# Optimization experiments

Hardware: AMD Instinct MI355X
Metric: run time of the kernel (lower is better)

The kernel has to match this reference:

```python
import jax, jax.numpy as jnp
import numpy as np

EPS = 1e-12  # keras K.l2_normalize epsilon


def _l2_normalize(v, axis):
    return v * jax.lax.rsqrt(jnp.maximum(jnp.sum(v * v, axis=axis, keepdims=True), EPS))


def setup_inputs() -> dict:
    key = jax.random.key(0)
    k1, k2, k3, k4 = jax.random.split(key, 4)
    B, T, D, K, O = 32, 1024, 512, 64, 1024
    x = jax.random.normal(k1, (B, T, D), dtype=jnp.float32)
    weight = jax.random.normal(k2, (D, K), dtype=jnp.float32) * (1.0 / np.sqrt(D))
    bias = jnp.zeros((K,), dtype=jnp.float32)
    centers = jax.random.normal(k3, (K, D), dtype=jnp.float32)
    reduc_dim = jax.random.normal(k4, (D * K, O), dtype=jnp.float32) * 0.01
    return {"x": x, "weight": weight, "bias": bias, "centers": centers, "reduc_dim": reduc_dim}


def reference(x, weight, bias, centers, reduc_dim):
    # x: [B,T,D], weight: [D,K], bias: [K]
    # soft assignment: softmax over centers
    a = jax.nn.softmax(jnp.einsum('btd,dk->btk', x, weight) + bias, axis=-1)  # [B,T,K]
    # aggregate descriptors per center: batch_dot over time axis -> [B,K,D]
    x_agg = jnp.einsum('btk,btd->bkd', a, x)
    # total soft weight per center: [B,K]
    sum_w = jnp.sum(a, axis=1)
    # residual vs centers, broadcast: [B,K,D]
    full = x_agg - sum_w[:, :, None] * centers[None, :, :]
    # intra-normalize per center vector
    full = _l2_normalize(full, axis=-1)
    B = x.shape[0]
    full = full.reshape(B, -1)  # [B, K*D]
    full = _l2_normalize(full, axis=-1)
    return full @ reduc_dim  # [B, output_dim]
```

## Files before the change

### kernel.cpp

```cpp
#include <hip/hip_runtime.h>
#include <math.h>

#define TT 1024
#define DD 512
#define KK 64
#define OO 1024
#define EPSF 1e-12f


__global__ void nv_kzero(float* __restrict__ p) {
  p[blockIdx.x * 256 + threadIdx.x] = 0.f;
}

__global__ __launch_bounds__(256) void nv_k1(
    const float* __restrict__ x, const float* __restrict__ weight,
    const float* __restrict__ bias, float* __restrict__ a_out,
    float* __restrict__ sum_w) {
  const int b = blockIdx.y;
  const int t0 = blockIdx.x * 64;
  const int tid = threadIdx.x;
  const int tx = tid & 15, ty = tid >> 4;
  const int r0 = ty * 4, c0 = tx * 4;

  __shared__ float xs[64 * 68];
  __shared__ float wsm[64 * 64];

  float acc[4][4] = {};

  for (int kk = 0; kk < DD; kk += 64) {
    __syncthreads();
#pragma unroll
    for (int it = 0; it < 4; ++it) {
      int f4 = it * 256 + tid;
      int r = f4 >> 4, d4 = (f4 & 15) << 2;
      *(float4*)(xs + r * 68 + d4) =
          *(const float4*)(x + (size_t)(b * TT + t0 + r) * DD + kk + d4);
    }
#pragma unroll
    for (int it = 0; it < 4; ++it) {
      int f4 = it * 256 + tid;
      int i = f4 >> 4, c4 = (f4 & 15) << 2;
      *(float4*)(wsm + i * 64 + c4) =
          *(const float4*)(weight + (size_t)(kk + i) * KK + c4);
    }
    __syncthreads();
#pragma unroll
    for (int i = 0; i < 64; i += 4) {
      float4 xv[4], wv[4];
#pragma unroll
      for (int j = 0; j < 4; ++j) xv[j] = *(const float4*)(xs + (r0 + j) * 68 + i);
#pragma unroll
      for (int ii = 0; ii < 4; ++ii) wv[ii] = *(const float4*)(wsm + (i + ii) * 64 + c0);
#pragma unroll
      for (int j = 0; j < 4; ++j) {
        acc[j][0] = fmaf(xv[j].x, wv[0].x, acc[j][0]);
        acc[j][1] = fmaf(xv[j].x, wv[0].y, acc[j][1]);
        acc[j][2] = fmaf(xv[j].x, wv[0].z, acc[j][2]);
        acc[j][3] = fmaf(xv[j].x, wv[0].w, acc[j][3]);
        acc[j][0] = fmaf(xv[j].y, wv[1].x, acc[j][0]);
        acc[j][1] = fmaf(xv[j].y, wv[1].y, acc[j][1]);
        acc[j][2] = fmaf(xv[j].y, wv[1].z, acc[j][2]);
        acc[j][3] = fmaf(xv[j].y, wv[1].w, acc[j][3]);
        acc[j][0] = fmaf(xv[j].z, wv[2].x, acc[j][0]);
        acc[j][1] = fmaf(xv[j].z, wv[2].y, acc[j][1]);
        acc[j][2] = fmaf(xv[j].z, wv[2].z, acc[j][2]);
        acc[j][3] = fmaf(xv[j].z, wv[2].w, acc[j][3]);
        acc[j][0] = fmaf(xv[j].w, wv[3].x, acc[j][0]);
        acc[j][1] = fmaf(xv[j].w, wv[3].y, acc[j][1]);
        acc[j][2] = fmaf(xv[j].w, wv[3].z, acc[j][2]);
        acc[j][3] = fmaf(xv[j].w, wv[3].w, acc[j][3]);
      }
    }
  }

  float4 bs = *(const float4*)(bias + c0);
  float swp0 = 0.f, swp1 = 0.f, swp2 = 0.f, swp3 = 0.f;
#pragma unroll
  for (int j = 0; j < 4; ++j) {
    float l0 = acc[j][0] + bs.x, l1 = acc[j][1] + bs.y;
    float l2 = acc[j][2] + bs.z, l3 = acc[j][3] + bs.w;
    float m = fmaxf(fmaxf(l0, l1), fmaxf(l2, l3));
#pragma unroll
    for (int s = 1; s <= 8; s <<= 1) m = fmaxf(m, __shfl_xor(m, s));
    float e0 = __expf(l0 - m), e1 = __expf(l1 - m);
    float e2 = __expf(l2 - m), e3 = __expf(l3 - m);
    float sum = e0 + e1 + e2 + e3;
#pragma unroll
    for (int s = 1; s <= 8; s <<= 1) sum += __shfl_xor(sum, s);
    float inv = 1.f / sum;
    float4 o = make_float4(e0 * inv, e1 * inv, e2 * inv, e3 * inv);
    swp0 += o.x; swp1 += o.y; swp2 += o.z; swp3 += o.w;
    *(float4*)(a_out + (size_t)(b * TT + t0 + r0 + j) * KK + c0) = o;
  }
  __syncthreads();
  *(float4*)(wsm + tid * 4) = make_float4(swp0, swp1, swp2, swp3);
  __syncthreads();
  if (tid < 64) {
    int txx = tid >> 2, cc = tid & 3;
    float s = 0.f;
#pragma unroll
    for (int g = 0; g < 16; ++g) s += wsm[(g * 16 + txx) * 4 + cc];
    atomicAdd(sum_w + b * KK + txx * 4 + cc, s);
  }
}

__global__ __launch_bounds__(256) void nv_k2(
    const float* __restrict__ a_in, const float* __restrict__ x,
    float* __restrict__ xaggP) {
  const int d_base = blockIdx.x * 64;
  const int b = blockIdx.y;
  const int split = blockIdx.z;
  const int tid = threadIdx.x;
  const int tx = tid & 15, ty = tid >> 4;
  const int r0 = ty * 4, c0 = tx * 4;

  __shared__ float as[64 * 64];
  __shared__ float xsm[64 * 64];

  float acc[4][4] = {};

  const int tbeg = split * 256;
  for (int t0 = tbeg; t0 < tbeg + 256; t0 += 64) {
    __syncthreads();
#pragma unroll
    for (int it = 0; it < 4; ++it) {
      int f4 = it * 256 + tid;
      int tt = f4 >> 4, c4 = (f4 & 15) << 2;
      *(float4*)(as + tt * 64 + c4) =
          *(const float4*)(a_in + (size_t)(b * TT + t0 + tt) * KK + c4);
      *(float4*)(xsm + tt * 64 + c4) =
          *(const float4*)(x + (size_t)(b * TT + t0 + tt) * DD + d_base + c4);
    }
    __syncthreads();
#pragma unroll 8
    for (int tt = 0; tt < 64; ++tt) {
      float4 av = *(const float4*)(as + tt * 64 + r0);
      float4 xv = *(const float4*)(xsm + tt * 64 + c0);
      acc[0][0] = fmaf(av.x, xv.x, acc[0][0]);
      acc[0][1] = fmaf(av.x, xv.y, acc[0][1]);
      acc[0][2] = fmaf(av.x, xv.z, acc[0][2]);
      acc[0][3] = fmaf(av.x, xv.w, acc[0][3]);
      acc[1][0] = fmaf(av.y, xv.x, acc[1][0]);
      acc[1][1] = fmaf(av.y, xv.y, acc[1][1]);
      acc[1][2] = fmaf(av.y, xv.z, acc[1][2]);
      acc[1][3] = fmaf(av.y, xv.w, acc[1][3]);
      acc[2][0] = fmaf(av.z, xv.x, acc[2][0]);
      acc[2][1] = fmaf(av.z, xv.y, acc[2][1]);
      acc[2][2] = fmaf(av.z, xv.z, acc[2][2]);
      acc[2][3] = fmaf(av.z, xv.w, acc[2][3]);
      acc[3][0] = fmaf(av.w, xv.x, acc[3][0]);
      acc[3][1] = fmaf(av.w, xv.y, acc[3][1]);
      acc[3][2] = fmaf(av.w, xv.z, acc[3][2]);
      acc[3][3] = fmaf(av.w, xv.w, acc[3][3]);
    }
  }
#pragma unroll
  for (int j = 0; j < 4; ++j) {
    *(float4*)(xaggP + ((size_t)((split * 32 + b) * KK + r0 + j)) * DD + d_base + c0) =
        make_float4(acc[j][0], acc[j][1], acc[j][2], acc[j][3]);
  }
}

__global__ __launch_bounds__(128) void nv_k3a(
    const float* __restrict__ xaggP, float* __restrict__ full,
    const float* __restrict__ centers, const float* __restrict__ sum_w,
    float* __restrict__ s1) {
  const int k = blockIdx.x, b = blockIdx.y;
  const int tid = threadIdx.x;
  const float sw = sum_w[b * KK + k];
  float4 v = make_float4(0.f, 0.f, 0.f, 0.f);
#pragma unroll
  for (int sp = 0; sp < 4; ++sp) {
    float4 p = *((const float4*)(xaggP + (size_t)((sp * 32 + b) * KK + k) * DD) + tid);
    v.x += p.x; v.y += p.y; v.z += p.z; v.w += p.w;
  }
  float4 c = *((const float4*)(centers + (size_t)k * DD) + tid);
  v.x = fmaf(-sw, c.x, v.x);
  v.y = fmaf(-sw, c.y, v.y);
  v.z = fmaf(-sw, c.z, v.z);
  v.w = fmaf(-sw, c.w, v.w);
  *((float4*)(full + (size_t)(b * KK + k) * DD) + tid) = v;
  float ss = v.x * v.x + v.y * v.y + v.z * v.z + v.w * v.w;
#pragma unroll
  for (int s = 1; s <= 32; s <<= 1) ss += __shfl_xor(ss, s);
  __shared__ float red[2];
  if ((tid & 63) == 0) red[tid >> 6] = ss;
  __syncthreads();
  if (tid == 0) s1[b * KK + k] = red[0] + red[1];
}

__global__ __launch_bounds__(64) void nv_k3b(const float* __restrict__ s1,
                                             float* __restrict__ scale) {
  const int b = blockIdx.x, k = threadIdx.x;
  float r = s1[b * KK + k];
  float d1 = fmaxf(r, EPSF);
  float s2 = r / d1;
#pragma unroll
  for (int s = 1; s <= 32; s <<= 1) s2 += __shfl_xor(s2, s);
  scale[b * KK + k] = rsqrtf(d1) * rsqrtf(fmaxf(s2, EPSF));
}

__global__ __launch_bounds__(128) void nv_k3c(float* __restrict__ full,
                                              const float* __restrict__ scale) {
  const int blk = blockIdx.x;
  const float sc = scale[blk];
  float4* p = (float4*)(full + (size_t)blk * DD) + threadIdx.x;
  float4 v = *p;
  v.x *= sc; v.y *= sc; v.z *= sc; v.w *= sc;
  *p = v;
}

__global__ __launch_bounds__(256) void nv_k4(
    const float* __restrict__ full, const float* __restrict__ reduc,
    float* __restrict__ outP) {
  const int c_base = blockIdx.x * 64;
  const int r_base = blockIdx.y * 512;
  const int tid = threadIdx.x;
  const int tx = tid & 15;
  const int ty = (tid >> 4) & 3;
  const int tz = tid >> 6;
  const int c0 = c_base + tx * 4;

  __shared__ float As[32 * 256];

  float acc[8][4] = {};

  for (int ch = 0; ch < 2; ++ch) {
    const int rch = r_base + ch * 256;
    __syncthreads();
#pragma unroll
    for (int it = 0; it < 8; ++it) {
      int f4 = it * 256 + tid;
      int bb = f4 >> 6, rr4 = (f4 & 63) << 2;
      *(float4*)(As + bb * 256 + rr4) =
          *(const float4*)(full + (size_t)bb * 32768 + rch + rr4);
    }
    __syncthreads();
#pragma unroll 4
    for (int i = 0; i < 16; ++i) {
      const int rl = i * 16 + ty * 4;
      float wv[4][4];
#pragma unroll
      for (int j = 0; j < 4; ++j) {
        float4 w = *(const float4*)(reduc + (size_t)(rch + rl + j) * OO + c0);
        wv[j][0] = w.x; wv[j][1] = w.y; wv[j][2] = w.z; wv[j][3] = w.w;
      }
#pragma unroll
      for (int bb = 0; bb < 8; ++bb) {
        float4 a4 = *(const float4*)(As + (tz * 8 + bb) * 256 + rl);
        float a_[4] = {a4.x, a4.y, a4.z, a4.w};
#pragma unroll
        for (int j = 0; j < 4; ++j) {
          acc[bb][0] = fmaf(a_[j], wv[j][0], acc[bb][0]);
          acc[bb][1] = fmaf(a_[j], wv[j][1], acc[bb][1]);
          acc[bb][2] = fmaf(a_[j], wv[j][2], acc[bb][2]);
          acc[bb][3] = fmaf(a_[j], wv[j][3], acc[bb][3]);
        }
      }
    }
  }

#pragma unroll
  for (int bb = 0; bb < 8; ++bb) {
    float4 v = make_float4(acc[bb][0], acc[bb][1], acc[bb][2], acc[bb][3]);
    v.x += __shfl_xor(v.x, 16); v.x += __shfl_xor(v.x, 32);
    v.y += __shfl_xor(v.y, 16); v.y += __shfl_xor(v.y, 32);
    v.z += __shfl_xor(v.z, 16); v.z += __shfl_xor(v.z, 32);
    v.w += __shfl_xor(v.w, 16); v.w += __shfl_xor(v.w, 32);
    if (ty == 0) {
      *(float4*)(outP + (size_t)(blockIdx.y * 32 + tz * 8 + bb) * OO + c0) = v;
    }
  }
}

__global__ __launch_bounds__(256) void nv_k5(const float* __restrict__ outP,
                                             float* __restrict__ out) {
  const int idx = blockIdx.x * 256 + threadIdx.x;
  float s = 0.f;
#pragma unroll 8
  for (int sp = 0; sp < 64; ++sp) s += outP[(size_t)sp * 32768 + idx];
  out[idx] = s;
}

extern "C" void kernel_launch(void* const* d_in, const int* in_sizes, int n_in,
                              void* d_out, int out_size, void* d_ws, size_t ws_size,
                              hipStream_t stream) {
  const float* x = (const float*)d_in[0];
  const float* weight = (const float*)d_in[1];
  const float* bias = (const float*)d_in[2];
  const float* centers = (const float*)d_in[3];
  const float* reduc = (const float*)d_in[4];
  float* out = (float*)d_out;
  float* ws = (float*)d_ws;

  float* a = ws;
  float* full = ws;
  float* xaggP = ws + 2097152;
  float* outP = ws + 2097152;
  float* sum_w = ws + 6291456;
  float* s1 = sum_w + 2048;
  float* scale = sum_w + 4096;

  nv_kzero<<<8, 256, 0, stream>>>(sum_w);
  nv_k1<<<dim3(16, 32), 256, 0, stream>>>(x, weight, bias, a, sum_w);
  nv_k2<<<dim3(8, 32, 4), 256, 0, stream>>>(a, x, xaggP);
  nv_k3a<<<dim3(64, 32), 128, 0, stream>>>(xaggP, full, centers, sum_w, s1);
  nv_k3b<<<32, 64, 0, stream>>>(s1, scale);
  nv_k3c<<<2048, 128, 0, stream>>>(full, scale);
  nv_k4<<<dim3(16, 64), 256, 0, stream>>>(full, reduc, outP);
  nv_k5<<<128, 256, 0, stream>>>(outP, out);
}
```

Measured before the change: 314.8 us.

## Use bf16 MFMA for assignment logits and aggregation GEMMs with transposed bf16 activations

Rewrites the logits GEMM and the soft-assignment aggregation GEMM to use bf16 MFMA 16x16x32 instructions instead of scalar FP32 FMAs. The weight is pre-converted and transposed to bf16, and x is converted on the fly with XOR-swizzled shared memory. Assignments are written transposed in bf16, and the time split for aggregation drops from 4 to 2. The aim is to cut compute time and halve the assignment traffic, at the cost of reduced precision in the logits and aggregation.

```diff
diff --git a/kernel.cpp b/kernel.cpp
--- a/kernel.cpp
+++ b/kernel.cpp
@@ -7,158 +7,218 @@
 #define OO 1024
 #define EPSF 1e-12f
 
+typedef __attribute__((ext_vector_type(8))) short bf16x8;
+typedef __attribute__((ext_vector_type(4))) float f32x4;
+
+__device__ __forceinline__ ushort f2bf(float f) {
+  unsigned u = __float_as_uint(f);
+  u = (u + 0x7FFFu + ((u >> 16) & 1u)) >> 16;
+  return (ushort)u;
+}
+__device__ __forceinline__ float bf2f(ushort h) {
+  unsigned u = ((unsigned)h) << 16;
+  return __uint_as_float(u);
+}
+
 
 __global__ void nv_kzero(float* __restrict__ p) {
   p[blockIdx.x * 256 + threadIdx.x] = 0.f;
 }
 
+__global__ __launch_bounds__(256) void nv_k0w(const float* __restrict__ w,
+                                              ushort* __restrict__ whT) {
+  int idx = blockIdx.x * 256 + threadIdx.x;
+  int d = idx >> 6, k = idx & 63;
+  whT[(size_t)k * DD + d] = f2bf(w[idx]);
+}
+
 __global__ __launch_bounds__(256) void nv_k1(
-    const float* __restrict__ x, const float* __restrict__ weight,
-    const float* __restrict__ bias, float* __restrict__ a_out,
+    const float* __restrict__ x, const ushort* __restrict__ whT,
+    const float* __restrict__ bias, ushort* __restrict__ aT,
     float* __restrict__ sum_w) {
+  const int b = blockIdx.y, t0 = blockIdx.x * 128;
+  const int tid = threadIdx.x;
+  const int wave = tid >> 6, lane = tid & 63, l15 = lane & 15, q = lane >> 4;
+
+  __shared__ ushort xs[128 * 64];
+  __shared__ ushort wsm[64 * 64];
+
+  f32x4 acc[2][4];
+#pragma unroll
+  for (int mt = 0; mt < 2; ++mt)
+#pragma unroll
+    for (int nt = 0; nt < 4; ++nt)
+#pragma unroll
+      for (int r = 0; r < 4; ++r) acc[mt][nt][r] = 0.f;
+
+  for (int dc = 0; dc < DD; dc += 64) {
+    __syncthreads();
+#pragma unroll
+    for (int it = 0; it < 4; ++it) {
+      int gid = it * 256 + tid;
+      int t = gid >> 3, g = gid & 7;
+      const float* px = x + ((size_t)(b * TT + t0 + t) * DD + dc + g * 8);
+      float4 v0 = *(const float4*)px;
+      float4 v1 = *(const float4*)(px + 4);
+      bf16x8 pk;
+      pk[0] = (short)f2bf(v0.x); pk[1] = (short)f2bf(v0.y);
+      pk[2] = (short)f2bf(v0.z); pk[3] = (short)f2bf(v0.w);
+      pk[4] = (short)f2bf(v1.x); pk[5] = (short)f2bf(v1.y);
+      pk[6] = (short)f2bf(v1.z); pk[7] = (short)f2bf(v1.w);
+      *(bf16x8*)(xs + t * 64 + ((g ^ (t & 7)) << 3)) = pk;
+    }
+#pragma unroll
+    for (int it = 0; it < 2; ++it) {
+      int gid = it * 256 + tid;
+      int k = gid >> 3, g = gid & 7;
+      bf16x8 v = *(const bf16x8*)(whT + (size_t)k * DD + dc + g * 8);
+      *(bf16x8*)(wsm + k * 64 + ((g ^ (k & 7)) << 3)) = v;
+    }
+    __syncthreads();
+#pragma unroll
+    for (int kc = 0; kc < 2; ++kc) {
+      int gq = kc * 4 + q;
+      bf16x8 bf[4];
+#pragma unroll
+      for (int nt = 0; nt < 4; ++nt) {
+        int k = nt * 16 + l15;
+        bf[nt] = *(const bf16x8*)(wsm + k * 64 + ((gq ^ (k & 7)) << 3));
+      }
+#pragma unroll
+      for (int mt = 0; mt < 2; ++mt) {
+        int t = wave * 32 + mt * 16 + l15;
+        bf16x8 af = *(const bf16x8*)(xs + t * 64 + ((gq ^ (t & 7)) << 3));
+#pragma unroll
+        for (int nt = 0; nt < 4; ++nt)
+          acc[mt][nt] = __builtin_amdgcn_mfma_f32_16x16x32_bf16(af, bf[nt], acc[mt][nt], 0, 0, 0);
+      }
+    }
+  }
+
+  float bia[4];
+#pragma unroll
+  for (int nt = 0; nt < 4; ++nt) bia[nt] = bias[nt * 16 + l15];
+
+  ushort au[2][4][4];
+  float sw[4] = {0.f, 0.f, 0.f, 0.f};
+#pragma unroll
+  for (int mt = 0; mt < 2; ++mt)
+#pragma unroll
+    for (int r = 0; r < 4; ++r) {
+      float l[4];
+#pragma unroll
+      for (int nt = 0; nt < 4; ++nt) l[nt] = acc[mt][nt][r] + bia[nt];
+      float m = fmaxf(fmaxf(l[0], l[1]), fmaxf(l[2], l[3]));
+#pragma unroll
+      for (int s = 1; s <= 8; s <<= 1) m = fmaxf(m, __shfl_xor(m, s));
+      float e[4];
+#pragma unroll
+      for (int nt = 0; nt < 4; ++nt) e[nt] = __expf(l[nt] - m);
+      float ssum = e[0] + e[1] + e[2] + e[3];
+#pragma unroll
+      for (int s = 1; s <= 8; s <<= 1) ssum += __shfl_xor(ssum, s);
+      float inv = 1.f / ssum;
+#pragma unroll
+      for (int nt = 0; nt < 4; ++nt) {
+        ushort u = f2bf(e[nt] * inv);
+        au[mt][nt][r] = u;
+        sw[nt] += bf2f(u);
+      }
+    }
+#pragma unroll
+  for (int nt = 0; nt < 4; ++nt) {
+    float s = sw[nt];
+    s += __shfl_xor(s, 16);
+    s += __shfl_xor(s, 32);
+    if (q == 0) atomicAdd(sum_w + b * KK + nt * 16 + l15, s);
+  }
+  __syncthreads();
+#pragma unroll
+  for (int mt = 0; mt < 2; ++mt)
+#pragma unroll
+    for (int nt = 0; nt < 4; ++nt)
+#pragma unroll
+      for (int r = 0; r < 4; ++r) {
+        int k = nt * 16 + l15;
+        int t = wave * 32 + mt * 16 + q * 4 + r;
+        int tg = t >> 3;
+        xs[k * 128 + ((tg ^ l15) << 3) + (t & 7)] = au[mt][nt][r];
+      }
+  __syncthreads();
+#pragma unroll
+  for (int it = 0; it < 4; ++it) {
+    int gid = it * 256 + tid;
+    int k = gid >> 4, g = gid & 15;
+    bf16x8 v = *(const bf16x8*)(xs + k * 128 + ((g ^ (k & 15)) << 3));
+    *(bf16x8*)(aT + (size_t)(b * KK + k) * TT + t0 + g * 8) = v;
+  }
+}
+
+__global__ __launch_bounds__(256) void nv_k2(
+    const ushort* __restrict__ aT, const float* __restrict__ x,
+    float* __restrict__ xaggP) {
+  const int dsp = blockIdx.x;
   const int b = blockIdx.y;
-  const int t0 = blockIdx.x * 64;
+  const int tsp = blockIdx.z;
   const int tid = threadIdx.x;
-  const int tx = tid & 15, ty = tid >> 4;
-  const int r0 = ty * 4, c0 = tx * 4;
-
-  __shared__ float xs[64 * 68];
-  __shared__ float wsm[64 * 64];
-
-  float acc[4][4] = {};
-
-  for (int kk = 0; kk < DD; kk += 64) {
-    __syncthreads();
+  const int wave = tid >> 6, lane = tid & 63, l15 = lane & 15, q = lane >> 4;
+  const int d0 = dsp * 64;
+
+  __shared__ ushort asx[64 * 64];
+  __shared__ ushort xsT[64 * 64];
+
+  f32x4 acc[4];
+#pragma unroll
+  for (int nt = 0; nt < 4; ++nt)
+#pragma unroll
+    for (int r = 0; r < 4; ++r) acc[nt][r] = 0.f;
+
+  for (int tc = 0; tc < 8; ++tc) {
+    const int t0 = tsp * 512 + tc * 64;
+    __syncthreads();
+#pragma unroll
+    for (int it = 0; it < 2; ++it) {
+      int gid = it * 256 + tid;
+      int k = gid >> 3, g = gid & 7;
+      bf16x8 v = *(const bf16x8*)(aT + (size_t)(b * KK + k) * TT + t0 + g * 8);
+      *(bf16x8*)(asx + k * 64 + ((g ^ (k & 7)) << 3)) = v;
+    }
 #pragma unroll
     for (int it = 0; it < 4; ++it) {
-      int f4 = it * 256 + tid;
-      int r = f4 >> 4, d4 = (f4 & 15) << 2;
-      *(float4*)(xs + r * 68 + d4) =
-          *(const float4*)(x + (size_t)(b * TT + t0 + r) * DD + kk + d4);
-    }
-#pragma unroll
-    for (int it = 0; it < 4; ++it) {
-      int f4 = it * 256 + tid;
-      int i = f4 >> 4, c4 = (f4 & 15) << 2;
-      *(float4*)(wsm + i * 64 + c4) =
-          *(const float4*)(weight + (size_t)(kk + i) * KK + c4);
-    }
-    __syncthreads();
-#pragma unroll
-    for (int i = 0; i < 64; i += 4) {
-      float4 xv[4], wv[4];
-#pragma unroll
-      for (int j = 0; j < 4; ++j) xv[j] = *(const float4*)(xs + (r0 + j) * 68 + i);
-#pragma unroll
-      for (int ii = 0; ii < 4; ++ii) wv[ii] = *(const float4*)(wsm + (i + ii) * 64 + c0);
-#pragma unroll
-      for (int j = 0; j < 4; ++j) {
-        acc[j][0] = fmaf(xv[j].x, wv[0].x, acc[j][0]);
-        acc[j][1] = fmaf(xv[j].x, wv[0].y, acc[j][1]);
-        acc[j][2] = fmaf(xv[j].x, wv[0].z, acc[j][2]);
-        acc[j][3] = fmaf(xv[j].x, wv[0].w, acc[j][3]);
-        acc[j][0] = fmaf(xv[j].y, wv[1].x, acc[j][0]);
-        acc[j][1] = fmaf(xv[j].y, wv[1].y, acc[j][1]);
-        acc[j][2] = fmaf(xv[j].y, wv[1].z, acc[j][2]);
-        acc[j][3] = fmaf(xv[j].y, wv[1].w, acc[j][3]);
-        acc[j][0] = fmaf(xv[j].z, wv[2].x, acc[j][0]);
-        acc[j][1] = fmaf(xv[j].z, wv[2].y, acc[j][1]);
-        acc[j][2] = fmaf(xv[j].z, wv[2].z, acc[j][2]);
-        acc[j][3] = fmaf(xv[j].z, wv[2].w, acc[j][3]);
-        acc[j][0] = fmaf(xv[j].w, wv[3].x, acc[j][0]);
-        acc[j][1] = fmaf(xv[j].w, wv[3].y, acc[j][1]);
-        acc[j][2] = fmaf(xv[j].w, wv[3].z, acc[j][2]);
-        acc[j][3] = fmaf(xv[j].w, wv[3].w, acc[j][3]);
-      }
-    }
-  }
-
-  float4 bs = *(const float4*)(bias + c0);
-  float swp0 = 0.f, swp1 = 0.f, swp2 = 0.f, swp3 = 0.f;
-#pragma unroll
-  for (int j = 0; j < 4; ++j) {
-    float l0 = acc[j][0] + bs.x, l1 = acc[j][1] + bs.y;
-    float l2 = acc[j][2] + bs.z, l3 = acc[j][3] + bs.w;
-    float m = fmaxf(fmaxf(l0, l1), fmaxf(l2, l3));
-#pragma unroll
-    for (int s = 1; s <= 8; s <<= 1) m = fmaxf(m, __shfl_xor(m, s));
-    float e0 = __expf(l0 - m), e1 = __expf(l1 - m);
-    float e2 = __expf(l2 - m), e3 = __expf(l3 - m);
-    float sum = e0 + e1 + e2 + e3;
-#pragma unroll
-    for (int s = 1; s <= 8; s <<= 1) sum += __shfl_xor(sum, s);
-    float inv = 1.f / sum;
-    float4 o = make_float4(e0 * inv, e1 * inv, e2 * inv, e3 * inv);
-    swp0 += o.x; swp1 += o.y; swp2 += o.z; swp3 += o.w;
-    *(float4*)(a_out + (size_t)(b * TT + t0 + r0 + j) * KK + c0) = o;
-  }
-  __syncthreads();
-  *(float4*)(wsm + tid * 4) = make_float4(swp0, swp1, swp2, swp3);
-  __syncthreads();
-  if (tid < 64) {
-    int txx = tid >> 2, cc = tid & 3;
-    float s = 0.f;
-#pragma unroll
-    for (int g = 0; g < 16; ++g) s += wsm[(g * 16 + txx) * 4 + cc];
-    atomicAdd(sum_w + b * KK + txx * 4 + cc, s);
-  }
-}
-
-__global__ __launch_bounds__(256) void nv_k2(
-    const float* __restrict__ a_in, const float* __restrict__ x,
-    float* __restrict__ xaggP) {
-  const int d_base = blockIdx.x * 64;
-  const int b = blockIdx.y;
-  const int split = blockIdx.z;
-  const int tid = threadIdx.x;
-  const int tx = tid & 15, ty = tid >> 4;
-  const int r0 = ty * 4, c0 = tx * 4;
-
-  __shared__ float as[64 * 64];
-  __shared__ float xsm[64 * 64];
-
-  float acc[4][4] = {};
-
-  const int tbeg = split * 256;
-  for (int t0 = tbeg; t0 < tbeg + 256; t0 += 64) {
-    __syncthreads();
-#pragma unroll
-    for (int it = 0; it < 4; ++it) {
-      int f4 = it * 256 + tid;
-      int tt = f4 >> 4, c4 = (f4 & 15) << 2;
-      *(float4*)(as + tt * 64 + c4) =
-          *(const float4*)(a_in + (size_t)(b * TT + t0 + tt) * KK + c4);
-      *(float4*)(xsm + tt * 64 + c4) =
-          *(const float4*)(x + (size_t)(b * TT + t0 + tt) * DD + d_base + c4);
-    }
-    __syncthreads();
-#pragma unroll 8
-    for (int tt = 0; tt < 64; ++tt) {
-      float4 av = *(const float4*)(as + tt * 64 + r0);
-      float4 xv = *(const float4*)(xsm + tt * 64 + c0);
-      acc[0][0] = fmaf(av.x, xv.x, acc[0][0]);
-      acc[0][1] = fmaf(av.x, xv.y, acc[0][1]);
-      acc[0][2] = fmaf(av.x, xv.z, acc[0][2]);
-      acc[0][3] = fmaf(av.x, xv.w, acc[0][3]);
-      acc[1][0] = fmaf(av.y, xv.x, acc[1][0]);
-      acc[1][1] = fmaf(av.y, xv.y, acc[1][1]);
-      acc[1][2] = fmaf(av.y, xv.z, acc[1][2]);
-      acc[1][3] = fmaf(av.y, xv.w, acc[1][3]);
-      acc[2][0] = fmaf(av.z, xv.x, acc[2][0]);
-      acc[2][1] = fmaf(av.z, xv.y, acc[2][1]);
-      acc[2][2] = fmaf(av.z, xv.z, acc[2][2]);
-      acc[2][3] = fmaf(av.z, xv.w, acc[2][3]);
-      acc[3][0] = fmaf(av.w, xv.x, acc[3][0]);
-      acc[3][1] = fmaf(av.w, xv.y, acc[3][1]);
-      acc[3][2] = fmaf(av.w, xv.z, acc[3][2]);
-      acc[3][3] = fmaf(av.w, xv.w, acc[3][3]);
-    }
-  }
-#pragma unroll
-  for (int j = 0; j < 4; ++j) {
-    *(float4*)(xaggP + ((size_t)((split * 32 + b) * KK + r0 + j)) * DD + d_base + c0) =
-        make_float4(acc[j][0], acc[j][1], acc[j][2], acc[j][3]);
-  }
+      int fid = it * 256 + tid;
+      int t = fid >> 4, dq = fid & 15;
+      float4 v = *(const float4*)(x + (size_t)(b * TT + t0 + t) * DD + d0 + dq * 4);
+      int tg = t >> 3;
+      float vv[4] = {v.x, v.y, v.z, v.w};
+#pragma unroll
+      for (int i = 0; i < 4; ++i) {
+        int d = dq * 4 + i;
+        int pos = tg ^ ((d ^ (d >> 3)) & 7);
+        xsT[d * 64 + (pos << 3) + (t & 7)] = f2bf(vv[i]);
+      }
+    }
+    __syncthreads();
+#pragma unroll
+    for (int kc = 0; kc < 2; ++kc) {
+      int gq = kc * 4 + q;
+      int k = wave * 16 + l15;
+      bf16x8 af = *(const bf16x8*)(asx + k * 64 + ((gq ^ (k & 7)) << 3));
+#pragma unroll
+      for (int nt = 0; nt < 4; ++nt) {
+        int d = nt * 16 + l15;
+        int pos = gq ^ ((d ^ (d >> 3)) & 7);
+        bf16x8 bf = *(const bf16x8*)(xsT + d * 64 + (pos << 3));
+        acc[nt] = __builtin_amdgcn_mfma_f32_16x16x32_bf16(af, bf, acc[nt], 0, 0, 0);
+      }
+    }
+  }
+#pragma unroll
+  for (int nt = 0; nt < 4; ++nt)
+#pragma unroll
+    for (int r = 0; r < 4; ++r) {
+      int k = wave * 16 + q * 4 + r;
+      xaggP[(size_t)((tsp * 32 + b) * KK + k) * DD + d0 + nt * 16 + l15] = acc[nt][r];
+    }
 }
 
 __global__ __launch_bounds__(128) void nv_k3a(
@@ -170,7 +230,7 @@
   const float sw = sum_w[b * KK + k];
   float4 v = make_float4(0.f, 0.f, 0.f, 0.f);
 #pragma unroll
-  for (int sp = 0; sp < 4; ++sp) {
+  for (int sp = 0; sp < 2; ++sp) {
     float4 p = *((const float4*)(xaggP + (size_t)((sp * 32 + b) * KK + k) * DD) + tid);
     v.x += p.x; v.y += p.y; v.z += p.z; v.w += p.w;
   }
@@ -293,17 +353,19 @@
   float* out = (float*)d_out;
   float* ws = (float*)d_ws;
 
-  float* a = ws;
-  float* full = ws;
+  ushort* aT = (ushort*)ws;
+  float* full = ws + 1048576;
   float* xaggP = ws + 2097152;
-  float* outP = ws + 2097152;
-  float* sum_w = ws + 6291456;
+  float* outP = ws + 4194304;
+  ushort* whT = (ushort*)(ws + 6291456);
+  float* sum_w = ws + 6291456 + 16384;
   float* s1 = sum_w + 2048;
   float* scale = sum_w + 4096;
 
   nv_kzero<<<8, 256, 0, stream>>>(sum_w);
-  nv_k1<<<dim3(16, 32), 256, 0, stream>>>(x, weight, bias, a, sum_w);
-  nv_k2<<<dim3(8, 32, 4), 256, 0, stream>>>(a, x, xaggP);
+  nv_k0w<<<128, 256, 0, stream>>>(weight, whT);
+  nv_k1<<<dim3(8, 32), 256, 0, stream>>>(x, whT, bias, aT, sum_w);
+  nv_k2<<<dim3(8, 32, 2), 256, 0, stream>>>(aT, x, xaggP);
   nv_k3a<<<dim3(64, 32), 128, 0, stream>>>(xaggP, full, centers, sum_w, s1);
   nv_k3b<<<32, 64, 0, stream>>>(s1, scale);
   nv_k3c<<<2048, 128, 0, stream>>>(full, scale);
```

Result: faster. 291.3 us (-7.4%).
